# Kernel optimization log

Measured on AMD Instinct MI355X. Metric: run time of the kernel, lower is better.

Reference implementation:

```python
import jax, jax.numpy as jnp
import numpy as np

N_LEVELS = 16
F_PER = 2
LOG2_HASH = 19
HASH_MASK = np.uint32(2 ** LOG2_HASH - 1)
BASE_RES = 16.0
FINEST_RES = 512.0
B_GROWTH = float(np.exp((np.log(FINEST_RES) - np.log(BASE_RES)) / (N_LEVELS - 1)))
PI = float(np.pi)
BOX_MIN = np.array([0.0, -PI, 0.5 * PI, -0.85 * PI], dtype=np.float32)
BOX_MAX = np.array([PI, PI, 0.85 * PI, -0.5 * PI], dtype=np.float32)
PRIMES = np.array([1, 2654435761, 805459861, 3674653429], dtype=np.uint32)
OFFSETS = np.array([[i, j, k, l] for i in (0, 1) for j in (0, 1)
                    for k in (0, 1) for l in (0, 1)], dtype=np.int32)  # (16,4)

BATCH = 131072


def setup_inputs() -> dict:
    key = jax.random.key(0)
    ks = jax.random.split(key, 16)
    bmin, bmax = jnp.asarray(BOX_MIN), jnp.asarray(BOX_MAX)
    u = jax.random.uniform(ks[0], (BATCH, 4), dtype=jnp.float32)
    x = bmin + u * (bmax - bmin)  # points inside the box
    tables = jax.random.uniform(ks[1], (N_LEVELS, 2 ** LOG2_HASH, F_PER),
                                minval=-1e-4, maxval=1e-4, dtype=jnp.float32)

    def lin(k, fi, fo):
        s = 1.0 / np.sqrt(fi)
        k1, k2 = jax.random.split(k)
        W = jax.random.uniform(k1, (fi, fo), minval=-s, maxval=s, dtype=jnp.float32)
        b = jax.random.uniform(k2, (fo,), minval=-s, maxval=s, dtype=jnp.float32)
        return W, b

    W1, b1 = lin(ks[2], 5, 512)
    W2, b2 = lin(ks[3], 512, 512)
    W3, b3 = lin(ks[4], 512, 512)
    W4, b4 = lin(ks[5], 512, 512)
    W5, b5 = lin(ks[6], 512, 512)
    W6, b6 = lin(ks[7], 512, 16)
    return dict(x=x, tables=tables, W1=W1, b1=b1, W2=W2, b2=b2, W3=W3, b3=b3,
                W4=W4, b4=b4, W5=W5, b5=b5, W6=W6, b6=b6)


def _forward(x, tables, W1, b1, W2, b2, W3, b3, W4, b4, W5, b5, W6, b6):
    bmin, bmax = jnp.asarray(BOX_MIN), jnp.asarray(BOX_MAX)
    primes = jnp.asarray(PRIMES)            # (4,) uint32
    offsets = jnp.asarray(OFFSETS)          # (16,4) int32
    B = x.shape[0]

    xc = jnp.clip(x, bmin, bmax)
    keep_mask = jnp.all(x == xc, axis=-1)   # (B,)

    resolutions = jnp.floor(BASE_RES * (B_GROWTH ** jnp.arange(N_LEVELS, dtype=jnp.float32)))

    def level_fn(_, lev):
        table, res = lev                     # table: (2^19, 2), res: scalar
        grid = (bmax - bmin) / res           # (4,)
        bl = jnp.floor((xc - bmin) / grid).astype(jnp.int32)      # (B,4) bottom-left voxel
        verts = (bl[:, None, :] + offsets[None]).astype(jnp.uint32)  # (B,16,4)
        h = verts * primes                   # uint32 wraparound multiply
        h = h[..., 0] ^ h[..., 1] ^ h[..., 2] ^ h[..., 3]
        idx = (h & HASH_MASK).astype(jnp.int32)                   # (B,16)
        emb = table[idx]                     # (B,16,2) gather
        # weight MLP on [resolution, x]
        feat = jnp.concatenate([jnp.broadcast_to(res, (B, 1)).astype(x.dtype), x], axis=1)  # (B,5)
        h1 = jax.nn.relu(feat @ W1 + b1)
        h2 = jax.nn.relu(h1 @ W2 + b2)
        h3 = jax.nn.relu(h2 @ W3 + b3)
        h4 = jax.nn.relu(h3 @ W4 + b4)
        h5 = jax.nn.relu(h4 @ W5 + b5)
        w = jax.nn.softmax(h5 @ W6 + b6, axis=1)                  # (B,16)
        out = jnp.einsum('bv,bvf->bf', w, emb)                    # (B,2)
        return None, out

    _, outs = jax.lax.scan(level_fn, None, (tables, resolutions))  # (L,B,2)
    out = jnp.moveaxis(outs, 0, 1).reshape(B, N_LEVELS * F_PER)    # (B,32)
    return out, keep_mask


def reference(x, tables, W1, b1, W2, b2, W3, b3, W4, b4, W5, b5, W6, b6):
    return _forward(x, tables, W1, b1, W2, b2, W3, b3, W4, b4, W5, b5, W6, b6)
```

## Files before the change

kernel.cpp:

```cpp
#include <hip/hip_runtime.h>
#include <stdint.h>

typedef unsigned int uint32;
typedef unsigned short u16;
typedef unsigned char u8;
typedef __attribute__((ext_vector_type(8))) int i32x8;
typedef __attribute__((ext_vector_type(16))) float f32x16;

#define HASH_BITS 19
#define TABLE_SZ (1u << HASH_BITS)
#define HMASK (TABLE_SZ - 1u)
#define PI_D 3.141592653589793
#define NPTS 131072
#define NWB4 (4 * 512 * 512)

#define MFMA64(A, B, C) __builtin_amdgcn_mfma_scale_f32_32x32x64_f8f6f4( \
    (A), (B), (C), 0, 0, 0, 0x7F7F7F7F, 0, 0x7F7F7F7F)

__device__ __forceinline__ u8 f2fp8(float f) {
    int r = __builtin_amdgcn_cvt_pk_fp8_f32(f, f, 0, false);
    return (u8)(r & 0xFF);
}

__device__ const float g_res[16] = {16.f,20.f,25.f,32.f,40.f,50.f,64.f,80.f,
                                    101.f,128.f,161.f,203.f,256.f,322.f,406.f,512.f};

__global__ void prep_weights(const float* __restrict__ W2, const float* __restrict__ W3,
                             const float* __restrict__ W4, const float* __restrict__ W5,
                             u8* __restrict__ wt8) {
    int pid = blockIdx.x * 256 + threadIdx.x;
    int e = pid * 2;
    if (e < NWB4) {
        int m = e >> 18;
        int rem = e & 262143;
        int n = rem >> 9, k = rem & 511;
        const float* W = (m == 0) ? W2 : (m == 1) ? W3 : (m == 2) ? W4 : W5;
        float v0 = W[k * 512 + n], v1 = W[(k + 1) * 512 + n];
        int g32 = n >> 5, l = (n & 31) + (((k >> 5) & 1) << 5), kk = k >> 6, j = k & 31;
        int dst = m * 262144 + g32 * 16384 + kk * 2048 + l * 32 + j;
        int pk = __builtin_amdgcn_cvt_pk_fp8_f32(v0, v1, 0, false);
        *(u16*)(wt8 + dst) = (u16)(pk & 0xFFFF);
    }
}

__global__ void mask_kernel(const float* __restrict__ x, float* __restrict__ mout, int B) {
    int i = blockIdx.x * 256 + threadIdx.x;
    if (i >= B) return;
    constexpr float bmin[4] = {0.0f, (float)(-PI_D), (float)(0.5 * PI_D), (float)(-0.85 * PI_D)};
    constexpr float bmax[4] = {(float)(PI_D), (float)(PI_D), (float)(0.85 * PI_D), (float)(-0.5 * PI_D)};
    float4 v = ((const float4*)x)[i];
    bool ok = (v.x >= bmin[0]) && (v.x <= bmax[0]) &&
              (v.y >= bmin[1]) && (v.y <= bmax[1]) &&
              (v.z >= bmin[2]) && (v.z <= bmax[2]) &&
              (v.w >= bmin[3]) && (v.w <= bmax[3]);
    mout[i] = ok ? 1.0f : 0.0f;
}

__global__ __launch_bounds__(512, 4)
void fused_mlp(const float* __restrict__ x, const float* __restrict__ tables,
               const float* __restrict__ W1, const float* __restrict__ b1,
               const u8* __restrict__ wt8, const float* __restrict__ W6,
               const float* __restrict__ b2, const float* __restrict__ b3,
               const float* __restrict__ b4, const float* __restrict__ b5,
               const float* __restrict__ b6, float* __restrict__ out, int level) {
    __shared__ u8 act[32768];
    __shared__ u8 w6lds[16384];
    __shared__ float xsh[64 * 4];
    __shared__ float swsh[64 * 17];

    const int tid = threadIdx.x;
    const int lane = tid & 63;
    const int wv = tid >> 6;
    const int pl = lane & 31;
    const int kh = lane >> 5;
    const int ptile = blockIdx.x;
    const float res = g_res[level];

    if (tid < 256) xsh[tid] = x[(size_t)ptile * 256 + tid];
    {
        int base = tid * 32;
#pragma unroll
        for (int i = 0; i < 32; ++i) {
            int d = base + i;
            int kk = d >> 11, l = (d >> 5) & 63, j = d & 31;
            int n = l & 31, k = kk * 64 + (l >> 5) * 32 + j;
            w6lds[d] = (n < 16) ? f2fp8(W6[k * 16 + n]) : (u8)0;
        }
    }
    __syncthreads();

    f32x16 acc00, acc01, acc10, acc11;

    {
        f32x16 zc = {0.f,0.f,0.f,0.f,0.f,0.f,0.f,0.f,0.f,0.f,0.f,0.f,0.f,0.f,0.f,0.f};
        float rs = res * (1.0f / 512.0f);
        i32x8 a1[2], bf[2];
#pragma unroll
        for (int ct = 0; ct < 2; ++ct) {
            int n = wv * 64 + ct * 32 + pl;
            uint32 w0 = 0, w1 = 0;
            if (kh == 0) {
                w0 = __builtin_amdgcn_cvt_pk_fp8_f32(W1[n] * 512.0f, W1[512 + n], 0, false);
                w0 = __builtin_amdgcn_cvt_pk_fp8_f32(W1[1024 + n], W1[1536 + n], w0, true);
                w1 = __builtin_amdgcn_cvt_pk_fp8_f32(W1[2048 + n], 0.0f, 0, false);
            }
            a1[ct] = (i32x8){(int)w0, (int)w1, 0, 0, 0, 0, 0, 0};
        }
#pragma unroll
        for (int rt = 0; rt < 2; ++rt) {
            float4 xv = *(const float4*)&xsh[(rt * 32 + pl) * 4];
            uint32 w0 = 0, w1 = 0;
            if (kh == 0) {
                w0 = __builtin_amdgcn_cvt_pk_fp8_f32(rs, xv.x, 0, false);
                w0 = __builtin_amdgcn_cvt_pk_fp8_f32(xv.y, xv.z, w0, true);
                w1 = __builtin_amdgcn_cvt_pk_fp8_f32(xv.w, 0.0f, 0, false);
            }
            bf[rt] = (i32x8){(int)w0, (int)w1, 0, 0, 0, 0, 0, 0};
        }
        acc00 = MFMA64(a1[0], bf[0], zc);
        acc01 = MFMA64(a1[1], bf[0], zc);
        acc10 = MFMA64(a1[0], bf[1], zc);
        acc11 = MFMA64(a1[1], bf[1], zc);
    }

#define EPI(ACC, RT, CT, BIASP) do {                                           \
        int nb = wv * 64 + (CT) * 32;                                          \
        _Pragma("unroll")                                                      \
        for (int q = 0; q < 4; ++q) {                                          \
            int nn = nb + q * 8 + 4 * kh;                                      \
            float4 bv = *(const float4*)&(BIASP)[nn];                          \
            float v0 = fmaxf((ACC)[q * 4 + 0] + bv.x, 0.f);                    \
            float v1 = fmaxf((ACC)[q * 4 + 1] + bv.y, 0.f);                    \
            float v2 = fmaxf((ACC)[q * 4 + 2] + bv.z, 0.f);                    \
            float v3 = fmaxf((ACC)[q * 4 + 3] + bv.w, 0.f);                    \
            uint32 wrd = __builtin_amdgcn_cvt_pk_fp8_f32(v0, v1, 0, false);    \
            wrd = __builtin_amdgcn_cvt_pk_fp8_f32(v2, v3, wrd, true);          \
            *(uint32*)&act[(RT) * 16384 + (wv * 2 + (CT)) * 1024 + pl * 32     \
                           + q * 8 + 4 * kh] = wrd;                            \
        }                                                                      \
    } while (0)

    EPI(acc00, 0, 0, b1); EPI(acc01, 0, 1, b1);
    EPI(acc10, 1, 0, b1); EPI(acc11, 1, 1, b1);
    __syncthreads();

#pragma unroll
    for (int ly = 0; ly < 4; ++ly) {
        const float* bias = (ly == 0) ? b2 : (ly == 1) ? b3 : (ly == 2) ? b4 : b5;
        const u8* lyb = wt8 + ly * 262144 + wv * 32768;
        f32x16 n00 = {0.f,0.f,0.f,0.f,0.f,0.f,0.f,0.f,0.f,0.f,0.f,0.f,0.f,0.f,0.f,0.f};
        f32x16 n01 = n00, n10 = n00, n11 = n00;
#pragma unroll
        for (int kk = 0; kk < 8; ++kk) {
            int koff = (kk * 2 + kh) * 1024 + pl * 32;
            i32x8 ba0 = *(const i32x8*)&act[koff];
            i32x8 ba1 = *(const i32x8*)&act[16384 + koff];
            i32x8 aw0 = *(const i32x8*)&lyb[kk * 2048 + lane * 32];
            i32x8 aw1 = *(const i32x8*)&lyb[16384 + kk * 2048 + lane * 32];
            n00 = MFMA64(aw0, ba0, n00);
            n10 = MFMA64(aw0, ba1, n10);
            n01 = MFMA64(aw1, ba0, n01);
            n11 = MFMA64(aw1, ba1, n11);
        }
        acc00 = n00; acc01 = n01; acc10 = n10; acc11 = n11;
        __syncthreads();
        EPI(acc00, 0, 0, bias); EPI(acc01, 0, 1, bias);
        EPI(acc10, 1, 0, bias); EPI(acc11, 1, 1, bias);
        __syncthreads();
    }

    if (wv < 2) {
        f32x16 a6 = {0.f,0.f,0.f,0.f,0.f,0.f,0.f,0.f,0.f,0.f,0.f,0.f,0.f,0.f,0.f,0.f};
#pragma unroll
        for (int kk = 0; kk < 8; ++kk) {
            i32x8 aw = *(const i32x8*)&w6lds[kk * 2048 + lane * 32];
            i32x8 ba = *(const i32x8*)&act[wv * 16384 + (kk * 2 + kh) * 1024 + pl * 32];
            a6 = MFMA64(aw, ba, a6);
        }
        int pt = wv * 32 + pl;
#pragma unroll
        for (int q = 0; q < 2; ++q) {
            int n0 = q * 8 + 4 * kh;
            float4 bv = *(const float4*)&b6[n0];
            swsh[pt * 17 + n0 + 0] = a6[q * 4 + 0] + bv.x;
            swsh[pt * 17 + n0 + 1] = a6[q * 4 + 1] + bv.y;
            swsh[pt * 17 + n0 + 2] = a6[q * 4 + 2] + bv.z;
            swsh[pt * 17 + n0 + 3] = a6[q * 4 + 3] + bv.w;
        }
    }
    __syncthreads();

    if (tid < 64) {
        float zv[16];
        float m = -1e30f;
#pragma unroll
        for (int j = 0; j < 16; ++j) { zv[j] = swsh[tid * 17 + j]; m = fmaxf(m, zv[j]); }
        float s = 0.f;
#pragma unroll
        for (int j = 0; j < 16; ++j) { zv[j] = expf(zv[j] - m); s += zv[j]; }
        float inv = 1.0f / s;
#pragma unroll
        for (int j = 0; j < 16; ++j) swsh[tid * 17 + j] = zv[j] * inv;
    }
    __syncthreads();

    {
        constexpr float bmin[4] = {0.0f, (float)(-PI_D), (float)(0.5 * PI_D), (float)(-0.85 * PI_D)};
        constexpr float bmax[4] = {(float)(PI_D), (float)(PI_D), (float)(0.85 * PI_D), (float)(-0.5 * PI_D)};
        constexpr uint32 primes[4] = {1u, 2654435761u, 805459861u, 3674653429u};
        const int p = tid >> 3;
        const int pr = tid & 7;
        uint32 ca[4], cb[4];
#pragma unroll
        for (int d = 0; d < 4; ++d) {
            float xv = xsh[p * 4 + d];
            float xc = fminf(fmaxf(xv, bmin[d]), bmax[d]);
            float g = (bmax[d] - bmin[d]) / res;
            float t = (xc - bmin[d]) / g;
            int bl = (int)floorf(t);
            ca[d] = (uint32)bl * primes[d];
            cb[d] = (uint32)(bl + 1) * primes[d];
        }
        float s0 = 0.f, s1 = 0.f;
        const float* tb = tables + (size_t)level * TABLE_SZ * 2;
#pragma unroll
        for (int vv = 0; vv < 2; ++vv) {
            int v = pr * 2 + vv;
            uint32 h = ((v & 8) ? cb[0] : ca[0]) ^ ((v & 4) ? cb[1] : ca[1]) ^
                       ((v & 2) ? cb[2] : ca[2]) ^ ((v & 1) ? cb[3] : ca[3]);
            float2 e = *(const float2*)(tb + (size_t)(h & HMASK) * 2);
            float wgt = swsh[p * 17 + v];
            s0 = fmaf(wgt, e.x, s0);
            s1 = fmaf(wgt, e.y, s1);
        }
#pragma unroll
        for (int sft = 1; sft < 8; sft <<= 1) {
            s0 += __shfl_xor(s0, sft, 64);
            s1 += __shfl_xor(s1, sft, 64);
        }
        if (pr == 0) {
            float* o = out + (size_t)(ptile * 64 + p) * 32 + level * 2;
            __builtin_nontemporal_store(s0, o);
            __builtin_nontemporal_store(s1, o + 1);
        }
    }
#undef EPI
}

extern "C" void kernel_launch(void* const* d_in, const int* in_sizes, int n_in,
                              void* d_out, int out_size, void* d_ws, size_t ws_size,
                              hipStream_t stream) {
    const float* x      = (const float*)d_in[0];
    const float* tables = (const float*)d_in[1];
    const float* W1 = (const float*)d_in[2];
    const float* b1 = (const float*)d_in[3];
    const float* W2 = (const float*)d_in[4];
    const float* b2 = (const float*)d_in[5];
    const float* W3 = (const float*)d_in[6];
    const float* b3 = (const float*)d_in[7];
    const float* W4 = (const float*)d_in[8];
    const float* b4 = (const float*)d_in[9];
    const float* W5 = (const float*)d_in[10];
    const float* b5 = (const float*)d_in[11];
    const float* W6 = (const float*)d_in[12];
    const float* b6 = (const float*)d_in[13];

    const int B = in_sizes[0] / 4;
    u8* wt8 = (u8*)d_ws;

    prep_weights<<<(NWB4 / 2 + 255) / 256, 256, 0, stream>>>(W2, W3, W4, W5, wt8);

    for (int level = 0; level < 16; ++level) {
        fused_mlp<<<dim3(NPTS / 64), 512, 0, stream>>>(
            x, tables, W1, b1, wt8, W6, b2, b3, b4, b5, b6, (float*)d_out, level);
    }
    mask_kernel<<<(B + 255) / 256, 256, 0, stream>>>(x, (float*)d_out + (size_t)B * 32, B);
}
```

Baseline: 3.241 ms.

## Prefetch hash-table gathers early and split LDS activation fragments to avoid bank conflicts

The hash computation and the random table gathers now run at the start of the kernel. Their results are stashed in LDS, so the global-memory latency overlaps with the MLP MFMA work instead of sitting at the tail. The activation and W6 LDS layouts are also reorganised so each MFMA operand is read as two 16-byte halves 512 bytes apart instead of one 32-byte strided read, which aims to cut LDS bank conflicts. This adds 8 KB of LDS per block, which may reduce occupancy, and ties the layout to matching index math in three places.

```diff
diff --git a/kernel.cpp b/kernel.cpp
--- a/kernel.cpp
+++ b/kernel.cpp
@@ -56,6 +56,13 @@
     mout[i] = ok ? 1.0f : 0.0f;
 }
 
+__device__ __forceinline__ i32x8 lds_frag(const u8* buf, int base) {
+    uint4 lo = *(const uint4*)&buf[base];
+    uint4 hi = *(const uint4*)&buf[base + 512];
+    return (i32x8){(int)lo.x, (int)lo.y, (int)lo.z, (int)lo.w,
+                   (int)hi.x, (int)hi.y, (int)hi.z, (int)hi.w};
+}
+
 __global__ __launch_bounds__(512, 4)
 void fused_mlp(const float* __restrict__ x, const float* __restrict__ tables,
                const float* __restrict__ W1, const float* __restrict__ b1,
@@ -67,6 +74,7 @@
     __shared__ u8 w6lds[16384];
     __shared__ float xsh[64 * 4];
     __shared__ float swsh[64 * 17];
+    __shared__ u8 elds[8192];
 
     const int tid = threadIdx.x;
     const int lane = tid & 63;
@@ -82,12 +90,41 @@
 #pragma unroll
         for (int i = 0; i < 32; ++i) {
             int d = base + i;
-            int kk = d >> 11, l = (d >> 5) & 63, j = d & 31;
-            int n = l & 31, k = kk * 64 + (l >> 5) * 32 + j;
-            w6lds[d] = (n < 16) ? f2fp8(W6[k * 16 + n]) : (u8)0;
-        }
-    }
-    __syncthreads();
+            int kunit = d >> 11, r = d & 2047, h2 = (r >> 9) & 3;
+            int pln = (r >> 4) & 31, jb = r & 15;
+            int k = kunit * 64 + (h2 >> 1) * 32 + (h2 & 1) * 16 + jb;
+            w6lds[d] = (pln < 16) ? f2fp8(W6[k * 16 + pln]) : (u8)0;
+        }
+    }
+    __syncthreads();
+
+    float2 e0v, e1v;
+    {
+        constexpr float bmin[4] = {0.0f, (float)(-PI_D), (float)(0.5 * PI_D), (float)(-0.85 * PI_D)};
+        constexpr float bmax[4] = {(float)(PI_D), (float)(PI_D), (float)(0.85 * PI_D), (float)(-0.5 * PI_D)};
+        constexpr uint32 primes[4] = {1u, 2654435761u, 805459861u, 3674653429u};
+        const int p = tid >> 3;
+        const int pr = tid & 7;
+        uint32 ca[4], cb[4];
+#pragma unroll
+        for (int d = 0; d < 4; ++d) {
+            float xv = xsh[p * 4 + d];
+            float xc = fminf(fmaxf(xv, bmin[d]), bmax[d]);
+            float g = (bmax[d] - bmin[d]) / res;
+            float t = (xc - bmin[d]) / g;
+            int bl = (int)floorf(t);
+            ca[d] = (uint32)bl * primes[d];
+            cb[d] = (uint32)(bl + 1) * primes[d];
+        }
+        const float* tb = tables + (size_t)level * TABLE_SZ * 2;
+        int v0 = pr * 2, v1 = pr * 2 + 1;
+        uint32 h0 = ((v0 & 8) ? cb[0] : ca[0]) ^ ((v0 & 4) ? cb[1] : ca[1]) ^
+                    ((v0 & 2) ? cb[2] : ca[2]) ^ ((v0 & 1) ? cb[3] : ca[3]);
+        uint32 h1 = ((v1 & 8) ? cb[0] : ca[0]) ^ ((v1 & 4) ? cb[1] : ca[1]) ^
+                    ((v1 & 2) ? cb[2] : ca[2]) ^ ((v1 & 1) ? cb[3] : ca[3]);
+        e0v = *(const float2*)(tb + (size_t)(h0 & HMASK) * 2);
+        e1v = *(const float2*)(tb + (size_t)(h1 & HMASK) * 2);
+    }
 
     f32x16 acc00, acc01, acc10, acc11;
 
@@ -135,13 +172,14 @@
             float v3 = fmaxf((ACC)[q * 4 + 3] + bv.w, 0.f);                    \
             uint32 wrd = __builtin_amdgcn_cvt_pk_fp8_f32(v0, v1, 0, false);    \
             wrd = __builtin_amdgcn_cvt_pk_fp8_f32(v2, v3, wrd, true);          \
-            *(uint32*)&act[(RT) * 16384 + (wv * 2 + (CT)) * 1024 + pl * 32     \
-                           + q * 8 + 4 * kh] = wrd;                            \
+            *(uint32*)&act[(RT) * 16384 + wv * 2048 + ((CT) * 2 + (q >> 1)) * 512 \
+                           + pl * 16 + (q & 1) * 8 + 4 * kh] = wrd;            \
         }                                                                      \
     } while (0)
 
     EPI(acc00, 0, 0, b1); EPI(acc01, 0, 1, b1);
     EPI(acc10, 1, 0, b1); EPI(acc11, 1, 1, b1);
+    *(float4*)&elds[tid * 16] = make_float4(e0v.x, e0v.y, e1v.x, e1v.y);
     __syncthreads();
 
 #pragma unroll
@@ -152,9 +190,9 @@
         f32x16 n01 = n00, n10 = n00, n11 = n00;
 #pragma unroll
         for (int kk = 0; kk < 8; ++kk) {
-            int koff = (kk * 2 + kh) * 1024 + pl * 32;
-            i32x8 ba0 = *(const i32x8*)&act[koff];
-            i32x8 ba1 = *(const i32x8*)&act[16384 + koff];
+            int rbase = kk * 2048 + kh * 1024 + pl * 16;
+            i32x8 ba0 = lds_frag(act, rbase);
+            i32x8 ba1 = lds_frag(act, 16384 + rbase);
             i32x8 aw0 = *(const i32x8*)&lyb[kk * 2048 + lane * 32];
             i32x8 aw1 = *(const i32x8*)&lyb[16384 + kk * 2048 + lane * 32];
             n00 = MFMA64(aw0, ba0, n00);
@@ -173,8 +211,9 @@
         f32x16 a6 = {0.f,0.f,0.f,0.f,0.f,0.f,0.f,0.f,0.f,0.f,0.f,0.f,0.f,0.f,0.f,0.f};
 #pragma unroll
         for (int kk = 0; kk < 8; ++kk) {
-            i32x8 aw = *(const i32x8*)&w6lds[kk * 2048 + lane * 32];
-            i32x8 ba = *(const i32x8*)&act[wv * 16384 + (kk * 2 + kh) * 1024 + pl * 32];
+            int rbase = kk * 2048 + kh * 1024 + pl * 16;
+            i32x8 aw = lds_frag(w6lds, rbase);
+            i32x8 ba = lds_frag(act, wv * 16384 + rbase);
             a6 = MFMA64(aw, ba, a6);
         }
         int pt = wv * 32 + pl;
@@ -205,34 +244,13 @@
     __syncthreads();
 
     {
-        constexpr float bmin[4] = {0.0f, (float)(-PI_D), (float)(0.5 * PI_D), (float)(-0.85 * PI_D)};
-        constexpr float bmax[4] = {(float)(PI_D), (float)(PI_D), (float)(0.85 * PI_D), (float)(-0.5 * PI_D)};
-        constexpr uint32 primes[4] = {1u, 2654435761u, 805459861u, 3674653429u};
         const int p = tid >> 3;
         const int pr = tid & 7;
-        uint32 ca[4], cb[4];
-#pragma unroll
-        for (int d = 0; d < 4; ++d) {
-            float xv = xsh[p * 4 + d];
-            float xc = fminf(fmaxf(xv, bmin[d]), bmax[d]);
-            float g = (bmax[d] - bmin[d]) / res;
-            float t = (xc - bmin[d]) / g;
-            int bl = (int)floorf(t);
-            ca[d] = (uint32)bl * primes[d];
-            cb[d] = (uint32)(bl + 1) * primes[d];
-        }
-        float s0 = 0.f, s1 = 0.f;
-        const float* tb = tables + (size_t)level * TABLE_SZ * 2;
-#pragma unroll
-        for (int vv = 0; vv < 2; ++vv) {
-            int v = pr * 2 + vv;
-            uint32 h = ((v & 8) ? cb[0] : ca[0]) ^ ((v & 4) ? cb[1] : ca[1]) ^
-                       ((v & 2) ? cb[2] : ca[2]) ^ ((v & 1) ? cb[3] : ca[3]);
-            float2 e = *(const float2*)(tb + (size_t)(h & HMASK) * 2);
-            float wgt = swsh[p * 17 + v];
-            s0 = fmaf(wgt, e.x, s0);
-            s1 = fmaf(wgt, e.y, s1);
-        }
+        float4 ev = *(const float4*)&elds[tid * 16];
+        float w0 = swsh[p * 17 + pr * 2];
+        float w1 = swsh[p * 17 + pr * 2 + 1];
+        float s0 = fmaf(w1, ev.z, fmaf(w0, ev.x, 0.f));
+        float s1 = fmaf(w1, ev.w, fmaf(w0, ev.y, 0.f));
 #pragma unroll
         for (int sft = 1; sft < 8; sft <<= 1) {
             s0 += __shfl_xor(s0, sft, 64);
```

New measurement: 3.737 ms. 15.3% more time.
